# Performance work log

Hardware: AMD Instinct MI355X
Metric: run time of the kernel (lower is better)

## Reference

```python
import jax, jax.numpy as jnp
import numpy as np

SEQ, PREV, BS, D_IN, H, D = 512, 512, 8, 1024, 16, 64


def setup_inputs() -> dict:
    key = jax.random.key(0)
    ks = jax.random.split(key, 10)
    s = 0.02
    inp = {
        "input_": jax.random.normal(ks[0], (SEQ, BS, D_IN), jnp.float32),
        "pos_embs": jax.random.normal(ks[1], (SEQ + PREV, D_IN), jnp.float32),
        "memory": jax.random.normal(ks[2], (PREV, BS, D_IN), jnp.float32),
        "u": jax.random.normal(ks[3], (H, D), jnp.float32) * s,
        "v": jax.random.normal(ks[4], (H, D), jnp.float32) * s,
        # causal mask allowing full attention to memory: triu with diagonal=1+prev
        "mask": (jnp.triu(jnp.ones((SEQ, SEQ + PREV), jnp.bool_), k=1 + PREV))[..., None],
        "W_kv": jax.random.normal(ks[5], (D_IN, 2 * H * D), jnp.float32) * s,
        "W_q": jax.random.normal(ks[6], (D_IN, H * D), jnp.float32) * s,
        "W_p": jax.random.normal(ks[7], (D_IN, H * D), jnp.float32) * s,
        "W_out": jax.random.normal(ks[8], (H * D, D_IN), jnp.float32) * s,
        "ln_gamma": jnp.ones((D_IN,), jnp.float32),
        "ln_beta": jnp.zeros((D_IN,), jnp.float32),
    }
    return inp


def _rel_shift(x):
    # x: (q, k, bs, H) -> pad one zero column, reshape-transpose trick, drop first row
    q, k, bs, h = x.shape
    zp = jnp.zeros((q, 1, bs, h), x.dtype)
    return jnp.concatenate([zp, x], axis=1).reshape(k + 1, q, bs, h)[1:].reshape(q, k, bs, h)


def reference(input_, pos_embs, memory, u, v, mask, W_kv, W_q, W_p, W_out, ln_gamma, ln_beta):
    cur_seq, bs, d_in = input_.shape
    prev_seq = memory.shape[0]
    tot = cur_seq + prev_seq
    h, d = u.shape
    scale = 1.0 / d ** 0.5

    iwm = jnp.concatenate([memory, input_], axis=0)          # (tot, bs, d_in)
    kv = jnp.einsum('jbe,ef->jbf', iwm, W_kv)                 # (tot, bs, 2*H*d)
    k_t, v_t = jnp.split(kv, 2, axis=-1)
    q_t = jnp.einsum('ibe,ef->ibf', input_, W_q)              # (cur, bs, H*d)

    q4 = q_t.reshape(cur_seq, bs, h, d)
    k4 = k_t.reshape(tot, bs, h, d)
    v4 = v_t.reshape(tot, bs, h, d)

    content_attn = jnp.einsum('ibhd,jbhd->ijbh', q4 + u, k4)  # (cur, tot, bs, H)

    p_t = (pos_embs @ W_p).reshape(tot, h, d)                 # (tot, H, d)
    position_attn = jnp.einsum('ibhd,jhd->ijbh', q4 + v, p_t)
    position_attn = _rel_shift(position_attn)

    attn = content_attn + position_attn
    attn = jnp.where(mask[..., None], -jnp.inf, attn)         # mask: (cur, tot, 1) -> (cur, tot, 1, 1)
    attn = jax.nn.softmax(attn * scale, axis=1)

    awv = jnp.einsum('ijbh,jbhd->ibhd', attn, v4).reshape(cur_seq, bs, h * d)
    out = input_ + awv @ W_out                                # residual

    mu = jnp.mean(out, axis=-1, keepdims=True)
    var = jnp.mean((out - mu) ** 2, axis=-1, keepdims=True)
    out = (out - mu) / jnp.sqrt(var + 1e-5) * ln_gamma + ln_beta
    return out
```

## Files before the change

### kernel.cpp

```cpp
#include <hip/hip_runtime.h>
#include <math.h>

#define SEQ  512
#define PREV 512
#define TOT  1024
#define BSZ  8
#define DIN  1024
#define NH   16
#define HD   64

typedef __bf16 bf16;
typedef __bf16 bf16x8 __attribute__((ext_vector_type(8)));
typedef float  f32x4  __attribute__((ext_vector_type(4)));
typedef float  f32x16 __attribute__((ext_vector_type(16)));
typedef unsigned int u32;
typedef u32 u32x2 __attribute__((ext_vector_type(2)));

__device__ __forceinline__ f32x4 MFMA16(bf16x8 a, bf16x8 b, f32x4 c) {
    return __builtin_amdgcn_mfma_f32_16x16x32_bf16(a, b, c, 0, 0, 0);
}
__device__ __forceinline__ f32x16 MFMA32(bf16x8 a, bf16x8 b, f32x16 c) {
    return __builtin_amdgcn_mfma_f32_32x32x16_bf16(a, b, c, 0, 0, 0);
}

#define GLOAD16(g, l) __builtin_amdgcn_global_load_lds( \
    (const __attribute__((address_space(1))) void*)(g), \
    (__attribute__((address_space(3))) void*)(l), 16, 0, 0)

__device__ __forceinline__ unsigned short bfbits(float x) {
    return __builtin_bit_cast(unsigned short, (bf16)x);
}
__device__ __forceinline__ float bf2f(u32 bits16) {
    return __builtin_bit_cast(float, bits16 << 16);
}

__global__ __launch_bounds__(256) void cast_all(
    const float* __restrict__ memory, const float* __restrict__ input_,
    const float* __restrict__ pos, bf16* __restrict__ iwm, bf16* __restrict__ posb)
{
    const int bid = blockIdx.x;
    const float* src; bf16* dst; int e4;
    if (bid < 8192) {
        e4 = (bid * 256 + threadIdx.x) * 4;
        src = (e4 < 4194304) ? memory : input_ - 4194304;
        dst = iwm;
    } else {
        e4 = ((bid - 8192) * 256 + threadIdx.x) * 4;
        src = pos; dst = posb;
    }
    float4 x = *(const float4*)(src + e4);
    union { bf16 h[4]; ushort4 u4; } pk;
    pk.h[0] = (bf16)x.x; pk.h[1] = (bf16)x.y; pk.h[2] = (bf16)x.z; pk.h[3] = (bf16)x.w;
    *(ushort4*)(dst + e4) = pk.u4;
}

__global__ __launch_bounds__(256) void transcast_all(
    const float* __restrict__ W_kv, const float* __restrict__ W_q,
    const float* __restrict__ W_p,  const float* __restrict__ W_out,
    bf16* __restrict__ wkv, bf16* __restrict__ wq,
    bf16* __restrict__ wp,  bf16* __restrict__ wo)
{
    __shared__ float tile[32][33];
    const int bx = blockIdx.x;
    const float* W; bf16* Wt; int N, bn;
    if (bx < 64)       { W = W_kv;  Wt = wkv; N = 2048; bn = bx * 32; }
    else if (bx < 96)  { W = W_q;   Wt = wq;  N = 1024; bn = (bx - 64) * 32; }
    else if (bx < 128) { W = W_p;   Wt = wp;  N = 1024; bn = (bx - 96) * 32; }
    else               { W = W_out; Wt = wo;  N = 1024; bn = (bx - 128) * 32; }
    const int t = threadIdx.x;
    const int bk = blockIdx.y * 32;
    const int r = t >> 3, c4 = (t & 7) * 4;
    float4 x = *(const float4*)(W + (size_t)(bk + r) * N + bn + c4);
    tile[r][c4 + 0] = x.x; tile[r][c4 + 1] = x.y;
    tile[r][c4 + 2] = x.z; tile[r][c4 + 3] = x.w;
    __syncthreads();
    union { bf16 h[4]; ushort4 u4; } pk;
#pragma unroll
    for (int i = 0; i < 4; ++i) pk.h[i] = (bf16)tile[c4 + i][r];
    *(ushort4*)(Wt + (size_t)(bn + r) * 1024 + bk + c4) = pk.u4;
}

__global__ __launch_bounds__(512, 1) void gemm_8ph(
    const bf16* __restrict__ A, const bf16* __restrict__ Bt,
    bf16* __restrict__ C, int M, int N, int K)
{
    __shared__ __align__(16) bf16 A_s[2][256 * 64];
    __shared__ __align__(16) bf16 B_s[2][256 * 64];
    const int t = threadIdx.x;
    const int w = t >> 6, lane = t & 63;
    const int li = lane & 15, hi = lane >> 4;
    const int wm = w >> 2, wn = w & 3;
    const int lin = blockIdx.y * 8 + blockIdx.x;
    const int xcd = lin & 7, idx = lin >> 3;
    const int bm = (xcd * 4 + (idx & 3)) * 256;
    const int bn = (idx >> 2) * 256;

    f32x4 acc[8][4];
#pragma unroll
    for (int m = 0; m < 8; ++m)
#pragma unroll
        for (int n = 0; n < 4; ++n) acc[m][n] = (f32x4){0.f, 0.f, 0.f, 0.f};

    auto stage_half = [&](int buf, int ks, int h) {
        const bf16* __restrict__ src = (h < 2) ? A : Bt;
        const int base = (h < 2) ? bm : bn;
        const int hh = (h & 1) * 128;
        bf16* dst = (h < 2) ? &A_s[buf][0] : &B_s[buf][0];
        const int k0 = ks << 6;
#pragma unroll
        for (int g = 0; g < 2; ++g) {
            const int row = hh + g * 64 + (t >> 3);
            const bf16* gp = src + (size_t)(base + row) * K + k0 + (((t & 7) ^ (row & 7)) * 8);
            GLOAD16(gp, dst + (size_t)(hh + g * 64 + w * 8) * 64);
        }
    };

    bf16x8 af[4], bfr[4];
    auto LDA = [&](int buf, int mh, int kk) {
#pragma unroll
        for (int m = 0; m < 4; ++m) {
            int row = wm * 128 + (mh * 4 + m) * 16 + li;
            af[m] = *(const bf16x8*)&A_s[buf][row * 64 + (((kk * 4 + hi) ^ (row & 7)) * 8)];
        }
    };
    auto LDB = [&](int buf, int kk) {
#pragma unroll
        for (int n = 0; n < 4; ++n) {
            int row = wn * 64 + n * 16 + li;
            bfr[n] = *(const bf16x8*)&B_s[buf][row * 64 + (((kk * 4 + hi) ^ (row & 7)) * 8)];
        }
    };

#define FMA_PHASE(mh)                                                    \
    asm volatile("s_waitcnt lgkmcnt(0)" ::: "memory");                   \
    __builtin_amdgcn_sched_barrier(0);                                   \
    __builtin_amdgcn_s_setprio(1);                                       \
    _Pragma("unroll")                                                    \
    for (int m = 0; m < 4; ++m)                                          \
        _Pragma("unroll")                                                \
        for (int n = 0; n < 4; ++n)                                      \
            acc[(mh) * 4 + m][n] = MFMA16(af[m], bfr[n], acc[(mh) * 4 + m][n]); \
    __builtin_amdgcn_s_setprio(0);                                       \
    __builtin_amdgcn_s_barrier();

    stage_half(0, 0, 0); stage_half(0, 0, 1); stage_half(0, 0, 2); stage_half(0, 0, 3);

    const int nk = K >> 6;
    for (int ks = 0; ks < nk; ++ks) {
        const int cur = ks & 1, nxt = cur ^ 1;
        const int ksn = (ks + 1 < nk) ? ks + 1 : ks;
        stage_half(nxt, ksn, 0);
        asm volatile("s_waitcnt vmcnt(2)" ::: "memory");
        __builtin_amdgcn_sched_barrier(0);
        __builtin_amdgcn_s_barrier();
        LDB(cur, 0); LDA(cur, 0, 0);
        FMA_PHASE(0)
        stage_half(nxt, ksn, 1);
        LDA(cur, 1, 0);
        FMA_PHASE(1)
        stage_half(nxt, ksn, 2);
        LDB(cur, 1); LDA(cur, 0, 1);
        FMA_PHASE(0)
        stage_half(nxt, ksn, 3);
        LDA(cur, 1, 1);
        FMA_PHASE(1)
    }
    asm volatile("s_waitcnt vmcnt(0)" ::: "memory");

#pragma unroll
    for (int m = 0; m < 8; ++m)
#pragma unroll
        for (int n = 0; n < 4; ++n)
#pragma unroll
            for (int r = 0; r < 4; ++r) {
                int row = bm + wm * 128 + m * 16 + hi * 4 + r;
                int col = bn + wn * 64 + n * 16 + li;
                C[(size_t)row * N + col] = (bf16)acc[m][n][r];
            }
#undef FMA_PHASE
}

template<int FOUT>
__global__ __launch_bounds__(256) void gemm_mfma(
    const bf16* __restrict__ A, const bf16* __restrict__ Bt,
    const float* __restrict__ Rres, bf16* __restrict__ Cb,
    float* __restrict__ Cf, int M, int N, int K)
{
    __shared__ __align__(16) bf16 A_s[128 * 64];
    __shared__ __align__(16) bf16 B_s[128 * 64];
    const int t = threadIdx.x;
    const int w = t >> 6, lane = t & 63;
    const int li = lane & 15, hi = lane >> 4;
    const int wr = w >> 1, wc = w & 1;
    const int bm = blockIdx.y * 128, bn = blockIdx.x * 128;
    const int l3 = lane >> 3, l7 = lane & 7;
    const int srcoct = ((l7 ^ l3) * 8);

    f32x4 acc[4][4];
#pragma unroll
    for (int m = 0; m < 4; ++m)
#pragma unroll
        for (int n = 0; n < 4; ++n) acc[m][n] = (f32x4){0.f, 0.f, 0.f, 0.f};

    auto stage = [&](int k0) {
#pragma unroll
        for (int i = 0; i < 4; ++i) {
            int c = w * 4 + i;
            const bf16* ga = A + (size_t)(bm + c * 8 + l3) * K + k0 + srcoct;
            GLOAD16(ga, &A_s[c * 512]);
            const bf16* gb = Bt + (size_t)(bn + c * 8 + l3) * K + k0 + srcoct;
            GLOAD16(gb, &B_s[c * 512]);
        }
    };

    stage(0);
    const int nk = K >> 6;
    for (int ks = 0; ks < nk; ++ks) {
        __syncthreads();
#pragma unroll
        for (int kk = 0; kk < 2; ++kk) {
            bf16x8 af[4], bfr[4];
#pragma unroll
            for (int m = 0; m < 4; ++m) {
                int row = wr * 64 + m * 16 + li;
                af[m] = *(const bf16x8*)&A_s[row * 64 + ((kk * 32 + hi * 8) ^ ((row & 7) * 8))];
            }
#pragma unroll
            for (int n = 0; n < 4; ++n) {
                int row = wc * 64 + n * 16 + li;
                bfr[n] = *(const bf16x8*)&B_s[row * 64 + ((kk * 32 + hi * 8) ^ ((row & 7) * 8))];
            }
#pragma unroll
            for (int m = 0; m < 4; ++m)
#pragma unroll
                for (int n = 0; n < 4; ++n)
                    acc[m][n] = MFMA16(af[m], bfr[n], acc[m][n]);
        }
        __syncthreads();
        if (ks + 1 < nk) stage((ks + 1) << 6);
    }

#pragma unroll
    for (int m = 0; m < 4; ++m)
#pragma unroll
        for (int n = 0; n < 4; ++n)
#pragma unroll
            for (int r = 0; r < 4; ++r) {
                int row = bm + wr * 64 + m * 16 + hi * 4 + r;
                int col = bn + wc * 64 + n * 16 + li;
                size_t off = (size_t)row * N + col;
                if (FOUT) Cf[off] = acc[m][n][r] + Rres[off];
                else      Cb[off] = (bf16)acc[m][n][r];
            }
}

__global__ __launch_bounds__(256, 2) void attn_mfma(
    const bf16* __restrict__ kv, const bf16* __restrict__ qb,
    const bf16* __restrict__ pb, const float* __restrict__ u,
    const float* __restrict__ v, bf16* __restrict__ awv)
{
    const int bi = (blockIdx.z & 1) ? (3 - blockIdx.x) : blockIdx.x;
    const int i0 = bi * 128;
    const int b  = blockIdx.y;
    const int h  = blockIdx.z;
    const int t  = threadIdx.x;
    const int w  = t >> 6;
    const int lane = t & 63;
    const int ql  = lane & 31;
    const int hi2 = lane >> 5;

    __shared__ __align__(16) bf16 K_s[64 * 64];
    __shared__ __align__(16) bf16 V_s[64][72];
    __shared__ __align__(16) bf16 P_s[256 * 64];
    __shared__ __align__(16) char SCR[4][6912];

    char* rsc = SCR[w];
    char* ps  = SCR[w];

    const int c8 = t & 7;
    const int rq = t >> 3;
    const int nt = 2 * bi + 10;
    const int C0 = 384 - i0;
    const float SCL = 0.125f * 1.44269504088896f;

    bf16x8 vreg[2];
#pragma unroll
    for (int p = 0; p < 2; ++p)
        vreg[p] = *(const bf16x8*)(kv + (size_t)((p * 32 + rq) * BSZ + b) * 2048 + 1024 + h * HD + c8 * 8);
#pragma unroll
    for (int p = 0; p < 2; ++p)
        GLOAD16(kv + (size_t)((p * 32 + rq) * BSZ + b) * 2048 + h * HD + ((c8 ^ (rq & 7)) * 8),
                K_s + (p * 32 + rq) * 64 + c8 * 8);
#pragma unroll
    for (int cp = 0; cp < 6; ++cp) {
        int grow = C0 + cp * 32 + rq;
        GLOAD16(pb + (size_t)grow * DIN + h * HD + ((c8 ^ (rq & 7)) * 8),
                P_s + (grow & 255) * 64 + c8 * 8);
    }

    bf16x8 qu[4], qv[4];
    {
        const size_t qoff = ((size_t)(i0 + w * 32 + ql) * BSZ + b) * DIN + h * HD;
#pragma unroll
        for (int kk = 0; kk < 4; ++kk) {
            bf16x8 q8 = *(const bf16x8*)(qb + qoff + kk * 16 + hi2 * 8);
            const float* up = u + h * HD + kk * 16 + hi2 * 8;
            const float* vp = v + h * HD + kk * 16 + hi2 * 8;
#pragma unroll
            for (int m = 0; m < 8; ++m) {
                float qf = (float)q8[m];
                qu[kk][m] = (bf16)(qf + up[m]);
                qv[kk][m] = (bf16)(qf + vp[m]);
            }
        }
    }

    float mrun = -1e30f, lrun = 0.f;
    f32x16 o[2];
    o[0] = (f32x16){}; o[1] = (f32x16){};

    const int phq = (31 - ql) & 3;
    const int sel = phq >> 1;
    const int shb = (phq & 1) * 16;

    for (int tt = 0; tt < nt; ++tt) {
        const int j0 = tt * 64;

        __builtin_amdgcn_s_barrier();
        __builtin_amdgcn_sched_barrier(0);

#pragma unroll
        for (int p = 0; p < 2; ++p) {
            int j = p * 32 + rq;
#pragma unroll
            for (int mm = 0; mm < 8; ++mm)
                V_s[c8 * 8 + mm][(j + 8 * c8) & 63] = vreg[p][mm];
        }
        asm volatile("s_waitcnt vmcnt(0) lgkmcnt(0)" ::: "memory");
        __builtin_amdgcn_sched_barrier(0);
        __builtin_amdgcn_s_barrier();
        __builtin_amdgcn_sched_barrier(0);

        f32x16 st[2];
        st[0] = (f32x16){}; st[1] = (f32x16){};
        __builtin_amdgcn_s_setprio(1);
#pragma unroll
        for (int jt = 0; jt < 2; ++jt) {
            int row = jt * 32 + ql;
#pragma unroll
            for (int kk = 0; kk < 4; ++kk) {
                bf16x8 kf = *(const bf16x8*)&K_s[row * 64 + (((kk * 2 + hi2) ^ (ql & 7)) * 8)];
                st[jt] = MFMA32(kf, qu[kk], st[jt]);
            }
        }
        const int bwg = j0 - i0 + 480 - 32 * w;
        f32x16 rp[3];
        rp[0] = (f32x16){}; rp[1] = (f32x16){}; rp[2] = (f32x16){};
#pragma unroll
        for (int Rt = 0; Rt < 3; ++Rt) {
            int ring = (bwg + Rt * 32 + ql) & 255;
#pragma unroll
            for (int kk = 0; kk < 4; ++kk) {
                bf16x8 pf = *(const bf16x8*)&P_s[ring * 64 + (((kk * 2 + hi2) ^ (ring & 7)) * 8)];
                rp[Rt] = MFMA32(pf, qv[kk], rp[Rt]);
            }
        }
        __builtin_amdgcn_s_setprio(0);

        __builtin_amdgcn_s_barrier();
        __builtin_amdgcn_sched_barrier(0);

        if (tt + 1 < nt) {
            const int j0n = j0 + 64;
#pragma unroll
            for (int p = 0; p < 2; ++p)
                vreg[p] = *(const bf16x8*)(kv + (size_t)((j0n + p * 32 + rq) * BSZ + b) * 2048 + 1024 + h * HD + c8 * 8);
#pragma unroll
            for (int p = 0; p < 2; ++p)
                GLOAD16(kv + (size_t)((j0n + p * 32 + rq) * BSZ + b) * 2048 + h * HD + ((c8 ^ (rq & 7)) * 8),
                        K_s + (p * 32 + rq) * 64 + c8 * 8);
        }
        if (tt + 3 < nt) {
            const int Cs = C0 + (tt + 3) * 64;
#pragma unroll
            for (int p = 0; p < 2; ++p) {
                int grow = Cs + p * 32 + rq;
                GLOAD16(pb + (size_t)grow * DIN + h * HD + ((c8 ^ (rq & 7)) * 8),
                        P_s + (grow & 255) * 64 + c8 * 8);
            }
        }

#pragma unroll
        for (int Rt = 0; Rt < 3; ++Rt)
#pragma unroll
            for (int a = 0; a < 4; ++a) {
                u32 lo = (u32)bfbits(rp[Rt][a * 4 + 0]) | ((u32)bfbits(rp[Rt][a * 4 + 1]) << 16);
                u32 hi = (u32)bfbits(rp[Rt][a * 4 + 2]) | ((u32)bfbits(rp[Rt][a * 4 + 3]) << 16);
                *(u32x2*)(rsc + ql * 216 + 64 * Rt + 16 * a + 8 * hi2) = (u32x2){lo, hi};
            }

        float rowmax = -1e30f;
        const int limb = i0 + 32 * w + ql + PREV - j0;
#pragma unroll
        for (int jt = 0; jt < 2; ++jt)
#pragma unroll
            for (int a = 0; a < 4; ++a) {
                int e = jt * 32 + 8 * a + 4 * hi2 + 31 - ql;
                const u32x2* W = (const u32x2*)(rsc + ql * 216 + 8 * (e >> 2));
                u32x2 A0 = W[0], A1 = W[1];
                u32 U0 = sel ? A0[1] : A0[0];
                u32 U1 = sel ? A1[0] : A0[1];
                u32 U2 = sel ? A1[1] : A1[0];
                u32 o0 = (u32)((((unsigned long long)U1 << 32) | U0) >> shb);
                u32 o1 = (u32)((((unsigned long long)U2 << 32) | U1) >> shb);
                float pq[4] = {bf2f(o0 & 0xffffu), bf2f(o0 >> 16),
                               bf2f(o1 & 0xffffu), bf2f(o1 >> 16)};
#pragma unroll
                for (int rr = 0; rr < 4; ++rr) {
                    int r = a * 4 + rr;
                    int lj = jt * 32 + 8 * a + 4 * hi2 + rr;
                    float sv = (st[jt][r] + pq[rr]) * SCL;
                    if (lj > limb) sv = -1e30f;
                    st[jt][r] = sv;
                    rowmax = fmaxf(rowmax, sv);
                }
            }
        rowmax = fmaxf(rowmax, __shfl_xor(rowmax, 32));

        if (!__all(rowmax - mrun <= 11.5f)) {
            float newm = fmaxf(mrun, rowmax);
            float fsc = exp2f(mrun - newm);
#pragma unroll
            for (int r = 0; r < 16; ++r) {
                float fr = __shfl(fsc, (r & 3) + 8 * (r >> 2) + 4 * hi2);
                o[0][r] *= fr; o[1][r] *= fr;
            }
            lrun *= fsc;
            mrun = newm;
        }
        float rowsum = 0.f;
#pragma unroll
        for (int jt = 0; jt < 2; ++jt)
#pragma unroll
            for (int r = 0; r < 16; ++r) {
                float p = exp2f(st[jt][r] - mrun);
                st[jt][r] = p;
                rowsum += p;
            }
        rowsum += __shfl_xor(rowsum, 32);
        lrun += rowsum;

#pragma unroll
        for (int jt = 0; jt < 2; ++jt)
#pragma unroll
            for (int a = 0; a < 4; ++a) {
                u32 lo = (u32)bfbits(st[jt][a * 4 + 0]) | ((u32)bfbits(st[jt][a * 4 + 1]) << 16);
                u32 hi = (u32)bfbits(st[jt][a * 4 + 2]) | ((u32)bfbits(st[jt][a * 4 + 3]) << 16);
                *(u32x2*)(ps + ql * 144 + 64 * jt + 16 * a + 8 * hi2) = (u32x2){lo, hi};
            }

        __builtin_amdgcn_s_setprio(1);
#pragma unroll
        for (int js = 0; js < 4; ++js) {
            bf16x8 pa = *(const bf16x8*)(ps + ql * 144 + 32 * js + 16 * hi2);
#pragma unroll
            for (int dt = 0; dt < 2; ++dt) {
                int dcol = dt * 32 + ql;
                int colb = (js * 16 + hi2 * 8 + 8 * (dcol >> 3)) & 63;
                bf16x8 vf = *(const bf16x8*)&V_s[dcol][colb];
                o[dt] = MFMA32(pa, vf, o[dt]);
            }
        }
        __builtin_amdgcn_s_setprio(0);
    }

    float lr[16];
#pragma unroll
    for (int r = 0; r < 16; ++r) lr[r] = __shfl(lrun, (r & 3) + 8 * (r >> 2) + 4 * hi2);
#pragma unroll
    for (int dt = 0; dt < 2; ++dt)
#pragma unroll
        for (int r = 0; r < 16; ++r) {
            int row = i0 + 32 * w + (r & 3) + 8 * (r >> 2) + 4 * hi2;
            awv[((size_t)row * BSZ + b) * DIN + h * HD + dt * 32 + ql] = (bf16)(o[dt][r] / lr[r]);
        }
}

__global__ __launch_bounds__(256) void ln_f32(
    float* __restrict__ out, const float* __restrict__ gamma, const float* __restrict__ beta)
{
    const int row = blockIdx.x;
    const int t = threadIdx.x;
    float4 x = *(float4*)(out + (size_t)row * DIN + t * 4);
    float s  = x.x + x.y + x.z + x.w;
    float ss = x.x * x.x + x.y * x.y + x.z * x.z + x.w * x.w;
#pragma unroll
    for (int wd = 1; wd < 64; wd <<= 1) { s += __shfl_xor(s, wd); ss += __shfl_xor(ss, wd); }
    __shared__ float sbuf[4], ssbuf[4];
    const int wave = t >> 6, lanei = t & 63;
    if (lanei == 0) { sbuf[wave] = s; ssbuf[wave] = ss; }
    __syncthreads();
    s  = sbuf[0] + sbuf[1] + sbuf[2] + sbuf[3];
    ss = ssbuf[0] + ssbuf[1] + ssbuf[2] + ssbuf[3];
    const float mu   = s * (1.f / DIN);
    const float var  = ss * (1.f / DIN) - mu * mu;
    const float rstd = rsqrtf(var + 1e-5f);
    float4 g  = *(const float4*)(gamma + t * 4);
    float4 bb = *(const float4*)(beta + t * 4);
    float4 y;
    y.x = (x.x - mu) * rstd * g.x + bb.x;
    y.y = (x.y - mu) * rstd * g.y + bb.y;
    y.z = (x.z - mu) * rstd * g.z + bb.z;
    y.w = (x.w - mu) * rstd * g.w + bb.w;
    *(float4*)(out + (size_t)row * DIN + t * 4) = y;
}

extern "C" void kernel_launch(void* const* d_in, const int* in_sizes, int n_in,
                              void* d_out, int out_size, void* d_ws, size_t ws_size,
                              hipStream_t stream)
{
    const float* input_ = (const float*)d_in[0];
    const float* pos    = (const float*)d_in[1];
    const float* memory = (const float*)d_in[2];
    const float* u      = (const float*)d_in[3];
    const float* v      = (const float*)d_in[4];
    const float* W_kv   = (const float*)d_in[6];
    const float* W_q    = (const float*)d_in[7];
    const float* W_p    = (const float*)d_in[8];
    const float* W_out  = (const float*)d_in[9];
    const float* gamma  = (const float*)d_in[10];
    const float* beta   = (const float*)d_in[11];

    bf16* iwm  = (bf16*)d_ws;
    bf16* kvb  = iwm  + (size_t)8192 * 1024;
    bf16* qbf  = kvb  + (size_t)8192 * 2048;
    bf16* pbf  = qbf  + (size_t)4096 * 1024;
    bf16* posb = pbf  + (size_t)1024 * 1024;
    bf16* wkv  = posb + (size_t)1024 * 1024;
    bf16* wq   = wkv  + (size_t)2048 * 1024;
    bf16* wp   = wq   + (size_t)1024 * 1024;
    bf16* wo   = wp   + (size_t)1024 * 1024;
    bf16* awvb = wo   + (size_t)1024 * 1024;
    float* outf = (float*)d_out;

    cast_all<<<9216, 256, 0, stream>>>(memory, input_, pos, iwm, posb);
    transcast_all<<<dim3(160, 32), 256, 0, stream>>>(W_kv, W_q, W_p, W_out, wkv, wq, wp, wo);

    gemm_8ph<<<dim3(8, 32), 512, 0, stream>>>(iwm, wkv, kvb, 8192, 2048, 1024);
    gemm_mfma<0><<<dim3(8, 32), 256, 0, stream>>>(iwm + (size_t)4096 * 1024, wq, nullptr, qbf, nullptr, 4096, 1024, 1024);
    gemm_mfma<0><<<dim3(8, 8),  256, 0, stream>>>(posb, wp, nullptr, pbf, nullptr, 1024, 1024, 1024);

    attn_mfma<<<dim3(4, 8, 16), 256, 0, stream>>>(kvb, qbf, pbf, u, v, awvb);

    gemm_mfma<1><<<dim3(8, 32), 256, 0, stream>>>(awvb, wo, input_, nullptr, outf, 4096, 1024, 1024);
    ln_f32<<<4096, 256, 0, stream>>>(outf, gamma, beta);
}
```

Measured before the change: 211.8 us.

## Merge prep kernels, restage KV GEMM pipeline, pass attention probs via permlane

Merges the activation cast kernel and the weight transpose-cast kernel into one launch. In the KV GEMM it drops the per-phase barriers and interleaved half-tile staging, and instead issues all four next-tile loads after one full vmcnt(0) wait and barrier. In attention, the softmax probabilities are repacked in registers with v_permlane32_swap instead of going through an LDS round trip. It also switches exp2 with a prescaled log2e to __expf, with a lower rescale threshold. The GEMM change gives up fine-grained load/compute interleaving in exchange for fewer barriers, and the softmax change alters numerics slightly.

```diff
diff --git a/kernel.cpp b/kernel.cpp
--- a/kernel.cpp
+++ b/kernel.cpp
@@ -34,41 +34,42 @@
     return __builtin_bit_cast(float, bits16 << 16);
 }
 
-__global__ __launch_bounds__(256) void cast_all(
+__global__ __launch_bounds__(256) void prep_all(
     const float* __restrict__ memory, const float* __restrict__ input_,
-    const float* __restrict__ pos, bf16* __restrict__ iwm, bf16* __restrict__ posb)
-{
-    const int bid = blockIdx.x;
-    const float* src; bf16* dst; int e4;
-    if (bid < 8192) {
-        e4 = (bid * 256 + threadIdx.x) * 4;
-        src = (e4 < 4194304) ? memory : input_ - 4194304;
-        dst = iwm;
-    } else {
-        e4 = ((bid - 8192) * 256 + threadIdx.x) * 4;
-        src = pos; dst = posb;
-    }
-    float4 x = *(const float4*)(src + e4);
-    union { bf16 h[4]; ushort4 u4; } pk;
-    pk.h[0] = (bf16)x.x; pk.h[1] = (bf16)x.y; pk.h[2] = (bf16)x.z; pk.h[3] = (bf16)x.w;
-    *(ushort4*)(dst + e4) = pk.u4;
-}
-
-__global__ __launch_bounds__(256) void transcast_all(
+    const float* __restrict__ pos,
     const float* __restrict__ W_kv, const float* __restrict__ W_q,
     const float* __restrict__ W_p,  const float* __restrict__ W_out,
+    bf16* __restrict__ iwm, bf16* __restrict__ posb,
     bf16* __restrict__ wkv, bf16* __restrict__ wq,
     bf16* __restrict__ wp,  bf16* __restrict__ wo)
 {
     __shared__ float tile[32][33];
-    const int bx = blockIdx.x;
+    const int bid = blockIdx.x;
+    const int t = threadIdx.x;
+    if (bid < 9216) {
+        const float* src; bf16* dst; int e4;
+        if (bid < 8192) {
+            e4 = (bid * 256 + t) * 4;
+            src = (e4 < 4194304) ? memory : input_ - 4194304;
+            dst = iwm;
+        } else {
+            e4 = ((bid - 8192) * 256 + t) * 4;
+            src = pos; dst = posb;
+        }
+        float4 x = *(const float4*)(src + e4);
+        union { bf16 h[4]; ushort4 u4; } pk;
+        pk.h[0] = (bf16)x.x; pk.h[1] = (bf16)x.y; pk.h[2] = (bf16)x.z; pk.h[3] = (bf16)x.w;
+        *(ushort4*)(dst + e4) = pk.u4;
+        return;
+    }
+    const int rem = bid - 9216;
+    const int bx = rem % 160, by = rem / 160;
     const float* W; bf16* Wt; int N, bn;
     if (bx < 64)       { W = W_kv;  Wt = wkv; N = 2048; bn = bx * 32; }
     else if (bx < 96)  { W = W_q;   Wt = wq;  N = 1024; bn = (bx - 64) * 32; }
     else if (bx < 128) { W = W_p;   Wt = wp;  N = 1024; bn = (bx - 96) * 32; }
     else               { W = W_out; Wt = wo;  N = 1024; bn = (bx - 128) * 32; }
-    const int t = threadIdx.x;
-    const int bk = blockIdx.y * 32;
+    const int bk = by * 32;
     const int r = t >> 3, c4 = (t & 7) * 4;
     float4 x = *(const float4*)(W + (size_t)(bk + r) * N + bn + c4);
     tile[r][c4 + 0] = x.x; tile[r][c4 + 1] = x.y;
@@ -140,32 +141,30 @@
         _Pragma("unroll")                                                \
         for (int n = 0; n < 4; ++n)                                      \
             acc[(mh) * 4 + m][n] = MFMA16(af[m], bfr[n], acc[(mh) * 4 + m][n]); \
-    __builtin_amdgcn_s_setprio(0);                                       \
-    __builtin_amdgcn_s_barrier();
+    __builtin_amdgcn_s_setprio(0);
 
     stage_half(0, 0, 0); stage_half(0, 0, 1); stage_half(0, 0, 2); stage_half(0, 0, 3);
 
     const int nk = K >> 6;
     for (int ks = 0; ks < nk; ++ks) {
         const int cur = ks & 1, nxt = cur ^ 1;
-        const int ksn = (ks + 1 < nk) ? ks + 1 : ks;
-        stage_half(nxt, ksn, 0);
-        asm volatile("s_waitcnt vmcnt(2)" ::: "memory");
+        asm volatile("s_waitcnt vmcnt(0)" ::: "memory");
         __builtin_amdgcn_sched_barrier(0);
         __builtin_amdgcn_s_barrier();
+        __builtin_amdgcn_sched_barrier(0);
+        if (ks + 1 < nk) {
+            stage_half(nxt, ks + 1, 0); stage_half(nxt, ks + 1, 1);
+            stage_half(nxt, ks + 1, 2); stage_half(nxt, ks + 1, 3);
+        }
         LDB(cur, 0); LDA(cur, 0, 0);
         FMA_PHASE(0)
-        stage_half(nxt, ksn, 1);
         LDA(cur, 1, 0);
         FMA_PHASE(1)
-        stage_half(nxt, ksn, 2);
         LDB(cur, 1); LDA(cur, 0, 1);
         FMA_PHASE(0)
-        stage_half(nxt, ksn, 3);
         LDA(cur, 1, 1);
         FMA_PHASE(1)
     }
-    asm volatile("s_waitcnt vmcnt(0)" ::: "memory");
 
 #pragma unroll
     for (int m = 0; m < 8; ++m)
@@ -275,13 +274,11 @@
     __shared__ __align__(16) char SCR[4][6912];
 
     char* rsc = SCR[w];
-    char* ps  = SCR[w];
 
     const int c8 = t & 7;
     const int rq = t >> 3;
     const int nt = 2 * bi + 10;
     const int C0 = 384 - i0;
-    const float SCL = 0.125f * 1.44269504088896f;
 
     bf16x8 vreg[2];
 #pragma unroll
@@ -419,7 +416,7 @@
                 for (int rr = 0; rr < 4; ++rr) {
                     int r = a * 4 + rr;
                     int lj = jt * 32 + 8 * a + 4 * hi2 + rr;
-                    float sv = (st[jt][r] + pq[rr]) * SCL;
+                    float sv = (st[jt][r] + pq[rr]) * 0.125f;
                     if (lj > limb) sv = -1e30f;
                     st[jt][r] = sv;
                     rowmax = fmaxf(rowmax, sv);
@@ -427,9 +424,9 @@
             }
         rowmax = fmaxf(rowmax, __shfl_xor(rowmax, 32));
 
-        if (!__all(rowmax - mrun <= 11.5f)) {
+        if (!__all(rowmax - mrun <= 8.f)) {
             float newm = fmaxf(mrun, rowmax);
-            float fsc = exp2f(mrun - newm);
+            float fsc = __expf(mrun - newm);
 #pragma unroll
             for (int r = 0; r < 16; ++r) {
                 float fr = __shfl(fsc, (r & 3) + 8 * (r >> 2) + 4 * hi2);
@@ -443,32 +440,38 @@
         for (int jt = 0; jt < 2; ++jt)
 #pragma unroll
             for (int r = 0; r < 16; ++r) {
-                float p = exp2f(st[jt][r] - mrun);
+                float p = __expf(st[jt][r] - mrun);
                 st[jt][r] = p;
                 rowsum += p;
             }
         rowsum += __shfl_xor(rowsum, 32);
         lrun += rowsum;
 
+        u32 pk0[2][4], pk1[2][4];
 #pragma unroll
         for (int jt = 0; jt < 2; ++jt)
 #pragma unroll
             for (int a = 0; a < 4; ++a) {
-                u32 lo = (u32)bfbits(st[jt][a * 4 + 0]) | ((u32)bfbits(st[jt][a * 4 + 1]) << 16);
-                u32 hi = (u32)bfbits(st[jt][a * 4 + 2]) | ((u32)bfbits(st[jt][a * 4 + 3]) << 16);
-                *(u32x2*)(ps + ql * 144 + 64 * jt + 16 * a + 8 * hi2) = (u32x2){lo, hi};
+                pk0[jt][a] = (u32)bfbits(st[jt][a * 4 + 0]) | ((u32)bfbits(st[jt][a * 4 + 1]) << 16);
+                pk1[jt][a] = (u32)bfbits(st[jt][a * 4 + 2]) | ((u32)bfbits(st[jt][a * 4 + 3]) << 16);
             }
 
         __builtin_amdgcn_s_setprio(1);
 #pragma unroll
         for (int js = 0; js < 4; ++js) {
-            bf16x8 pa = *(const bf16x8*)(ps + ql * 144 + 32 * js + 16 * hi2);
+            const int jt = js >> 1, a0 = 2 * (js & 1), a1 = a0 + 1;
+            u32 w0 = pk0[jt][a0], w2 = pk0[jt][a1];
+            asm("v_permlane32_swap_b32 %0, %1" : "+v"(w0), "+v"(w2));
+            u32 w1 = pk1[jt][a0], w3 = pk1[jt][a1];
+            asm("v_permlane32_swap_b32 %0, %1" : "+v"(w1), "+v"(w3));
+            union { u32 uw[4]; bf16x8 vv; } pa;
+            pa.uw[0] = w0; pa.uw[1] = w1; pa.uw[2] = w2; pa.uw[3] = w3;
 #pragma unroll
             for (int dt = 0; dt < 2; ++dt) {
                 int dcol = dt * 32 + ql;
                 int colb = (js * 16 + hi2 * 8 + 8 * (dcol >> 3)) & 63;
                 bf16x8 vf = *(const bf16x8*)&V_s[dcol][colb];
-                o[dt] = MFMA32(pa, vf, o[dt]);
+                o[dt] = MFMA32(pa.vv, vf, o[dt]);
             }
         }
         __builtin_amdgcn_s_setprio(0);
@@ -543,8 +546,8 @@
     bf16* awvb = wo   + (size_t)1024 * 1024;
     float* outf = (float*)d_out;
 
-    cast_all<<<9216, 256, 0, stream>>>(memory, input_, pos, iwm, posb);
-    transcast_all<<<dim3(160, 32), 256, 0, stream>>>(W_kv, W_q, W_p, W_out, wkv, wq, wp, wo);
+    prep_all<<<14336, 256, 0, stream>>>(memory, input_, pos, W_kv, W_q, W_p, W_out,
+                                        iwm, posb, wkv, wq, wp, wo);
 
     gemm_8ph<<<dim3(8, 32), 512, 0, stream>>>(iwm, wkv, kvb, 8192, 2048, 1024);
     gemm_mfma<0><<<dim3(8, 32), 256, 0, stream>>>(iwm + (size_t)4096 * 1024, wq, nullptr, qbf, nullptr, 4096, 1024, 1024);
```

Result: faster. 192.2 us (-9.3%).
